# Optimization experiments

Hardware: AMD Instinct MI355X
Metric: run time of the kernel (lower is better)

Reference implementation:

```python
import jax, jax.numpy as jnp
import numpy as np

N, D, H = 524288, 64, 256


def setup_inputs() -> dict:
    key = jax.random.key(0)
    k1, k2, k3 = jax.random.split(key, 3)
    X = jax.random.normal(k1, (N, D), dtype=jnp.float32)
    centers = jax.random.normal(k2, (H, D), dtype=jnp.float32)
    w = jax.random.normal(k3, (1, H), dtype=jnp.float32) / np.sqrt(H)
    b = jnp.zeros((1,), dtype=jnp.float32)
    return {"X": X, "centers": centers, "w": w, "b": b}


def reference(X, centers, w, b):
    # RBF feature map: phi[n, h] = exp(-||X[n] - centers[h]||^2)
    # Squared euclidean distance via the expanded form to avoid the
    # [N, H, D] broadcast intermediate the naive torch version builds.
    x2 = jnp.sum(X * X, axis=-1, keepdims=True)           # [N, 1]
    c2 = jnp.sum(centers * centers, axis=-1)               # [H]
    xc = jnp.einsum('nd,hd->nh', X, centers)               # [N, H]
    d2 = jnp.maximum(x2 - 2.0 * xc + c2[None, :], 0.0)     # [N, H]
    feats = jnp.exp(-d2)                                   # gaussian kernel
    # Linear head: nn.Linear(hidden_dim, 1)
    return feats @ w.T + b                                 # [N, 1]
```

## Files before the change

kernel.cpp:

```cpp
#include <hip/hip_runtime.h>

#define NROWS 524288
#define DDIM  64
#define HCENT 256
#define GRID  512
#define CPB   4

typedef short bf16x8 __attribute__((ext_vector_type(8)));
typedef float f32x4  __attribute__((ext_vector_type(4)));

#define LOG2E 1.4426950408889634f
#define K2L   2.8853900817779268f
#define BIASF 80.0f

__device__ __forceinline__ float fast_exp2(float x) {
#if __has_builtin(__builtin_amdgcn_exp2f)
  return __builtin_amdgcn_exp2f(x);
#else
  return exp2f(x);
#endif
}

__global__ __launch_bounds__(512, 4) void rbf_main(const float* __restrict__ X,
                                                   const float* __restrict__ bptr,
                                                   const float* __restrict__ centers,
                                                   const float* __restrict__ w,
                                                   float* __restrict__ out) {
  __shared__ int4 BH[16 * 2 * 64];
  __shared__ int4 BL[16 * 2 * 64];
  __shared__ float2 CWs[HCENT];

  const int tid  = threadIdx.x;
  const int wave = tid >> 6;
  const int lane = tid & 63;
  const int q    = lane >> 4;
  const int c    = lane & 15;

  float c2acc[2] = {0.f, 0.f};
#pragma unroll
  for (int i = 0; i < 4; ++i) {
    int pair = wave * 4 + i;
    int ct = pair >> 1;
    int kc = pair & 1;
    const float* src = centers + (ct * 16 + c) * DDIM + kc * 32 + q * 8;
    float4 f0 = reinterpret_cast<const float4*>(src)[0];
    float4 f1 = reinterpret_cast<const float4*>(src)[1];
    float xs[8] = {f0.x, f0.y, f0.z, f0.w, f1.x, f1.y, f1.z, f1.w};
    int hp[4], lp[4];
    float part = 0.f;
#pragma unroll
    for (int p = 0; p < 4; ++p) {
      float x0 = xs[2 * p], x1 = xs[2 * p + 1];
      part = fmaf(x0, x0, part);
      part = fmaf(x1, x1, part);
      unsigned u0 = __float_as_uint(x0);
      unsigned u1 = __float_as_uint(x1);
      float l0 = x0 - __uint_as_float(u0 & 0xFFFF0000u);
      float l1 = x1 - __uint_as_float(u1 & 0xFFFF0000u);
      hp[p] = (int)((u1 & 0xFFFF0000u) | (u0 >> 16));
      lp[p] = (int)((__float_as_uint(l1) & 0xFFFF0000u) | (__float_as_uint(l0) >> 16));
    }
    part += __shfl_xor(part, 16, 64);
    part += __shfl_xor(part, 32, 64);
    c2acc[i >> 1] += part;
    int idx = pair * 64 + lane;
    BH[idx] = make_int4(hp[0], hp[1], hp[2], hp[3]);
    BL[idx] = make_int4(lp[0], lp[1], lp[2], lp[3]);
  }
  if (lane < 16) {
#pragma unroll
    for (int t = 0; t < 2; ++t) {
      int h = (wave * 2 + t) * 16 + lane;
      CWs[h] = make_float2(-fmaf(c2acc[t], LOG2E, BIASF), w[h]);
    }
  }

  float bval = bptr[0];

  __syncthreads();

  const bf16x8* BHv = reinterpret_cast<const bf16x8*>(BH);
  const bf16x8* BLv = reinterpret_cast<const bf16x8*>(BL);

#pragma unroll 1
  for (int s = 0; s < CPB; ++s) {
    int rowbase = (blockIdx.x * CPB + s) * 256 + wave * 32;

    bf16x8 ah[2][2], al[2][2];
    float x2p[2];
#pragma unroll
    for (int rt = 0; rt < 2; ++rt) {
      const float* rp = X + (rowbase + rt * 16 + c) * DDIM + q * 8;
      float part = 0.f;
#pragma unroll
      for (int kc = 0; kc < 2; ++kc) {
        float4 f0 = reinterpret_cast<const float4*>(rp + kc * 32)[0];
        float4 f1 = reinterpret_cast<const float4*>(rp + kc * 32)[1];
        float xs[8] = {f0.x, f0.y, f0.z, f0.w, f1.x, f1.y, f1.z, f1.w};
        union { int i[4]; bf16x8 v; } uh, ul;
#pragma unroll
        for (int p = 0; p < 4; ++p) {
          float x0 = xs[2 * p], x1 = xs[2 * p + 1];
          part = fmaf(x0, x0, part);
          part = fmaf(x1, x1, part);
          unsigned u0 = __float_as_uint(x0);
          unsigned u1 = __float_as_uint(x1);
          float l0 = x0 - __uint_as_float(u0 & 0xFFFF0000u);
          float l1 = x1 - __uint_as_float(u1 & 0xFFFF0000u);
          uh.i[p] = (int)((u1 & 0xFFFF0000u) | (u0 >> 16));
          ul.i[p] = (int)((__float_as_uint(l1) & 0xFFFF0000u) | (__float_as_uint(l0) >> 16));
        }
        ah[rt][kc] = uh.v;
        al[rt][kc] = ul.v;
      }
      x2p[rt] = part;
    }

    float psum[2][4] = {{0.f, 0.f, 0.f, 0.f}, {0.f, 0.f, 0.f, 0.f}};
#pragma unroll 2
    for (int ct = 0; ct < 16; ++ct) {
      int idx = ct * 128 + lane;
      bf16x8 bh0 = BHv[idx], bh1 = BHv[idx + 64];
      bf16x8 bl0 = BLv[idx], bl1 = BLv[idx + 64];
      float2 mw = CWs[ct * 16 + c];
#pragma unroll
      for (int rt = 0; rt < 2; ++rt) {
        f32x4 acc = {0.f, 0.f, 0.f, 0.f};
        acc = __builtin_amdgcn_mfma_f32_16x16x32_bf16(ah[rt][0], bh0, acc, 0, 0, 0);
        acc = __builtin_amdgcn_mfma_f32_16x16x32_bf16(ah[rt][1], bh1, acc, 0, 0, 0);
        acc = __builtin_amdgcn_mfma_f32_16x16x32_bf16(al[rt][0], bh0, acc, 0, 0, 0);
        acc = __builtin_amdgcn_mfma_f32_16x16x32_bf16(al[rt][1], bh1, acc, 0, 0, 0);
        acc = __builtin_amdgcn_mfma_f32_16x16x32_bf16(ah[rt][0], bl0, acc, 0, 0, 0);
        acc = __builtin_amdgcn_mfma_f32_16x16x32_bf16(ah[rt][1], bl1, acc, 0, 0, 0);
#pragma unroll
        for (int r = 0; r < 4; ++r) {
          float e = fast_exp2(fmaf(acc[r], K2L, mw.x));
          psum[rt][r] = fmaf(e, mw.y, psum[rt][r]);
        }
      }
    }

#pragma unroll
    for (int rt = 0; rt < 2; ++rt) {
      float part = x2p[rt];
      part += __shfl_xor(part, 16, 64);
      part += __shfl_xor(part, 32, 64);
#pragma unroll
      for (int r = 0; r < 4; ++r) {
        float v = psum[rt][r];
        v += __shfl_xor(v, 1, 64);
        v += __shfl_xor(v, 2, 64);
        v += __shfl_xor(v, 4, 64);
        v += __shfl_xor(v, 8, 64);
        float x2row = __shfl(part, q * 4 + r, 64);
        float rowf = fast_exp2(fmaf(-LOG2E, x2row, BIASF));
        psum[rt][r] = fmaf(v, rowf, bval);
      }
      if (c == 0) {
        float4 o = make_float4(psum[rt][0], psum[rt][1], psum[rt][2], psum[rt][3]);
        *reinterpret_cast<float4*>(out + rowbase + rt * 16 + q * 4) = o;
      }
    }
  }
}

extern "C" void kernel_launch(void* const* d_in, const int* in_sizes, int n_in,
                              void* d_out, int out_size, void* d_ws, size_t ws_size,
                              hipStream_t stream) {
  const float* X       = (const float*)d_in[0];
  const float* centers = (const float*)d_in[1];
  const float* w       = (const float*)d_in[2];
  const float* b       = (const float*)d_in[3];
  float* out = (float*)d_out;
  (void)d_ws; (void)ws_size;

  rbf_main<<<GRID, 512, 0, stream>>>(X, b, centers, w, out);
}
```

Before: 206.4 us.

## Switch to single fp16 MFMA pass and software-prefetch next row chunk

Replaces the split-bf16 three-term emulation (hi*hi, lo*hi, hi*lo, six MFMAs per tile) with a single fp16 conversion of X and centers, two MFMAs per tile. This drops the low-part LDS buffer and its conversion work. It also unrolls the four chunks and double-buffers the raw X loads, so the next chunk's global loads overlap the current chunk's compute. fp16 loses mantissa bits versus the split scheme and can overflow for large inputs, which risks accuracy in the exponent of the gaussian.

```diff
diff --git a/kernel.cpp b/kernel.cpp
--- a/kernel.cpp
+++ b/kernel.cpp
@@ -6,8 +6,8 @@
 #define GRID  512
 #define CPB   4
 
-typedef short bf16x8 __attribute__((ext_vector_type(8)));
-typedef float f32x4  __attribute__((ext_vector_type(4)));
+typedef _Float16 half8 __attribute__((ext_vector_type(8)));
+typedef float    f32x4 __attribute__((ext_vector_type(4)));
 
 #define LOG2E 1.4426950408889634f
 #define K2L   2.8853900817779268f
@@ -25,9 +25,104 @@
                                                    const float* __restrict__ bptr,
                                                    const float* __restrict__ centers,
                                                    const float* __restrict__ w,
+                                                   float* __restrict__ out);
+
+__device__ __forceinline__ void load_chunk(const float* __restrict__ X, int rowbase,
+                                           int c, int q, float4 (&raw)[8]) {
+#pragma unroll
+  for (int rt = 0; rt < 2; ++rt) {
+    const float* rp = X + (rowbase + rt * 16 + c) * DDIM + q * 8;
+#pragma unroll
+    for (int kc = 0; kc < 2; ++kc) {
+      raw[rt * 4 + kc * 2 + 0] = reinterpret_cast<const float4*>(rp + kc * 32)[0];
+      raw[rt * 4 + kc * 2 + 1] = reinterpret_cast<const float4*>(rp + kc * 32)[1];
+    }
+  }
+}
+
+__device__ __forceinline__ void convert_chunk(const float4 (&raw)[8],
+                                              half8 (&a)[2][2], float (&x2p)[2]) {
+#pragma unroll
+  for (int rt = 0; rt < 2; ++rt) {
+    float part = 0.f;
+#pragma unroll
+    for (int kc = 0; kc < 2; ++kc) {
+      const float4 f0 = raw[rt * 4 + kc * 2 + 0];
+      const float4 f1 = raw[rt * 4 + kc * 2 + 1];
+      const float xs[8] = {f0.x, f0.y, f0.z, f0.w, f1.x, f1.y, f1.z, f1.w};
+      union { _Float16 h[8]; half8 v; } u;
+#pragma unroll
+      for (int p = 0; p < 8; ++p) {
+        part = fmaf(xs[p], xs[p], part);
+        u.h[p] = (_Float16)xs[p];
+      }
+      a[rt][kc] = u.v;
+    }
+    x2p[rt] = part;
+  }
+}
+
+__device__ __forceinline__ void chunk_body(const float* __restrict__ X, int rowbase,
+                                           bool prefetch,
+                                           const float4 (&cur)[8], float4 (&nxt)[8],
+                                           const half8* __restrict__ BHv,
+                                           const float2* __restrict__ CWs,
+                                           int lane, int q, int c, float bval,
+                                           float* __restrict__ out) {
+  if (prefetch) load_chunk(X, rowbase + 256, c, q, nxt);
+
+  half8 a[2][2];
+  float x2p[2];
+  convert_chunk(cur, a, x2p);
+
+  float psum[2][4] = {{0.f, 0.f, 0.f, 0.f}, {0.f, 0.f, 0.f, 0.f}};
+#pragma unroll 2
+  for (int ct = 0; ct < 16; ++ct) {
+    int idx = ct * 128 + lane;
+    half8 bh0 = BHv[idx], bh1 = BHv[idx + 64];
+    float2 mw = CWs[ct * 16 + c];
+#pragma unroll
+    for (int rt = 0; rt < 2; ++rt) {
+      f32x4 acc = {0.f, 0.f, 0.f, 0.f};
+      acc = __builtin_amdgcn_mfma_f32_16x16x32_f16(a[rt][0], bh0, acc, 0, 0, 0);
+      acc = __builtin_amdgcn_mfma_f32_16x16x32_f16(a[rt][1], bh1, acc, 0, 0, 0);
+#pragma unroll
+      for (int r = 0; r < 4; ++r) {
+        float e = fast_exp2(fmaf(acc[r], K2L, mw.x));
+        psum[rt][r] = fmaf(e, mw.y, psum[rt][r]);
+      }
+    }
+  }
+
+#pragma unroll
+  for (int rt = 0; rt < 2; ++rt) {
+    float part = x2p[rt];
+    part += __shfl_xor(part, 16, 64);
+    part += __shfl_xor(part, 32, 64);
+#pragma unroll
+    for (int r = 0; r < 4; ++r) {
+      float v = psum[rt][r];
+      v += __shfl_xor(v, 1, 64);
+      v += __shfl_xor(v, 2, 64);
+      v += __shfl_xor(v, 4, 64);
+      v += __shfl_xor(v, 8, 64);
+      float x2row = __shfl(part, q * 4 + r, 64);
+      float rowf = fast_exp2(fmaf(-LOG2E, x2row, BIASF));
+      psum[rt][r] = fmaf(v, rowf, bval);
+    }
+    if (c == 0) {
+      float4 o = make_float4(psum[rt][0], psum[rt][1], psum[rt][2], psum[rt][3]);
+      *reinterpret_cast<float4*>(out + rowbase + rt * 16 + q * 4) = o;
+    }
+  }
+}
+
+__global__ __launch_bounds__(512, 4) void rbf_main(const float* __restrict__ X,
+                                                   const float* __restrict__ bptr,
+                                                   const float* __restrict__ centers,
+                                                   const float* __restrict__ w,
                                                    float* __restrict__ out) {
   __shared__ int4 BH[16 * 2 * 64];
-  __shared__ int4 BL[16 * 2 * 64];
   __shared__ float2 CWs[HCENT];
 
   const int tid  = threadIdx.x;
@@ -45,27 +140,18 @@
     const float* src = centers + (ct * 16 + c) * DDIM + kc * 32 + q * 8;
     float4 f0 = reinterpret_cast<const float4*>(src)[0];
     float4 f1 = reinterpret_cast<const float4*>(src)[1];
-    float xs[8] = {f0.x, f0.y, f0.z, f0.w, f1.x, f1.y, f1.z, f1.w};
-    int hp[4], lp[4];
+    const float xs[8] = {f0.x, f0.y, f0.z, f0.w, f1.x, f1.y, f1.z, f1.w};
+    union { _Float16 h[8]; int4 i4; } u;
     float part = 0.f;
 #pragma unroll
-    for (int p = 0; p < 4; ++p) {
-      float x0 = xs[2 * p], x1 = xs[2 * p + 1];
-      part = fmaf(x0, x0, part);
-      part = fmaf(x1, x1, part);
-      unsigned u0 = __float_as_uint(x0);
-      unsigned u1 = __float_as_uint(x1);
-      float l0 = x0 - __uint_as_float(u0 & 0xFFFF0000u);
-      float l1 = x1 - __uint_as_float(u1 & 0xFFFF0000u);
-      hp[p] = (int)((u1 & 0xFFFF0000u) | (u0 >> 16));
-      lp[p] = (int)((__float_as_uint(l1) & 0xFFFF0000u) | (__float_as_uint(l0) >> 16));
+    for (int p = 0; p < 8; ++p) {
+      part = fmaf(xs[p], xs[p], part);
+      u.h[p] = (_Float16)xs[p];
     }
     part += __shfl_xor(part, 16, 64);
     part += __shfl_xor(part, 32, 64);
     c2acc[i >> 1] += part;
-    int idx = pair * 64 + lane;
-    BH[idx] = make_int4(hp[0], hp[1], hp[2], hp[3]);
-    BL[idx] = make_int4(lp[0], lp[1], lp[2], lp[3]);
+    BH[pair * 64 + lane] = u.i4;
   }
   if (lane < 16) {
 #pragma unroll
@@ -79,89 +165,17 @@
 
   __syncthreads();
 
-  const bf16x8* BHv = reinterpret_cast<const bf16x8*>(BH);
-  const bf16x8* BLv = reinterpret_cast<const bf16x8*>(BL);
+  const half8* BHv = reinterpret_cast<const half8*>(BH);
 
-#pragma unroll 1
-  for (int s = 0; s < CPB; ++s) {
-    int rowbase = (blockIdx.x * CPB + s) * 256 + wave * 32;
+  const int rb0 = blockIdx.x * CPB * 256 + wave * 32;
 
-    bf16x8 ah[2][2], al[2][2];
-    float x2p[2];
-#pragma unroll
-    for (int rt = 0; rt < 2; ++rt) {
-      const float* rp = X + (rowbase + rt * 16 + c) * DDIM + q * 8;
-      float part = 0.f;
-#pragma unroll
-      for (int kc = 0; kc < 2; ++kc) {
-        float4 f0 = reinterpret_cast<const float4*>(rp + kc * 32)[0];
-        float4 f1 = reinterpret_cast<const float4*>(rp + kc * 32)[1];
-        float xs[8] = {f0.x, f0.y, f0.z, f0.w, f1.x, f1.y, f1.z, f1.w};
-        union { int i[4]; bf16x8 v; } uh, ul;
-#pragma unroll
-        for (int p = 0; p < 4; ++p) {
-          float x0 = xs[2 * p], x1 = xs[2 * p + 1];
-          part = fmaf(x0, x0, part);
-          part = fmaf(x1, x1, part);
-          unsigned u0 = __float_as_uint(x0);
-          unsigned u1 = __float_as_uint(x1);
-          float l0 = x0 - __uint_as_float(u0 & 0xFFFF0000u);
-          float l1 = x1 - __uint_as_float(u1 & 0xFFFF0000u);
-          uh.i[p] = (int)((u1 & 0xFFFF0000u) | (u0 >> 16));
-          ul.i[p] = (int)((__float_as_uint(l1) & 0xFFFF0000u) | (__float_as_uint(l0) >> 16));
-        }
-        ah[rt][kc] = uh.v;
-        al[rt][kc] = ul.v;
-      }
-      x2p[rt] = part;
-    }
+  float4 rawA[8], rawB[8];
+  load_chunk(X, rb0, c, q, rawA);
 
-    float psum[2][4] = {{0.f, 0.f, 0.f, 0.f}, {0.f, 0.f, 0.f, 0.f}};
-#pragma unroll 2
-    for (int ct = 0; ct < 16; ++ct) {
-      int idx = ct * 128 + lane;
-      bf16x8 bh0 = BHv[idx], bh1 = BHv[idx + 64];
-      bf16x8 bl0 = BLv[idx], bl1 = BLv[idx + 64];
-      float2 mw = CWs[ct * 16 + c];
-#pragma unroll
-      for (int rt = 0; rt < 2; ++rt) {
-        f32x4 acc = {0.f, 0.f, 0.f, 0.f};
-        acc = __builtin_amdgcn_mfma_f32_16x16x32_bf16(ah[rt][0], bh0, acc, 0, 0, 0);
-        acc = __builtin_amdgcn_mfma_f32_16x16x32_bf16(ah[rt][1], bh1, acc, 0, 0, 0);
-        acc = __builtin_amdgcn_mfma_f32_16x16x32_bf16(al[rt][0], bh0, acc, 0, 0, 0);
-        acc = __builtin_amdgcn_mfma_f32_16x16x32_bf16(al[rt][1], bh1, acc, 0, 0, 0);
-        acc = __builtin_amdgcn_mfma_f32_16x16x32_bf16(ah[rt][0], bl0, acc, 0, 0, 0);
-        acc = __builtin_amdgcn_mfma_f32_16x16x32_bf16(ah[rt][1], bl1, acc, 0, 0, 0);
-#pragma unroll
-        for (int r = 0; r < 4; ++r) {
-          float e = fast_exp2(fmaf(acc[r], K2L, mw.x));
-          psum[rt][r] = fmaf(e, mw.y, psum[rt][r]);
-        }
-      }
-    }
-
-#pragma unroll
-    for (int rt = 0; rt < 2; ++rt) {
-      float part = x2p[rt];
-      part += __shfl_xor(part, 16, 64);
-      part += __shfl_xor(part, 32, 64);
-#pragma unroll
-      for (int r = 0; r < 4; ++r) {
-        float v = psum[rt][r];
-        v += __shfl_xor(v, 1, 64);
-        v += __shfl_xor(v, 2, 64);
-        v += __shfl_xor(v, 4, 64);
-        v += __shfl_xor(v, 8, 64);
-        float x2row = __shfl(part, q * 4 + r, 64);
-        float rowf = fast_exp2(fmaf(-LOG2E, x2row, BIASF));
-        psum[rt][r] = fmaf(v, rowf, bval);
-      }
-      if (c == 0) {
-        float4 o = make_float4(psum[rt][0], psum[rt][1], psum[rt][2], psum[rt][3]);
-        *reinterpret_cast<float4*>(out + rowbase + rt * 16 + q * 4) = o;
-      }
-    }
-  }
+  chunk_body(X, rb0 + 0 * 256, true,  rawA, rawB, BHv, CWs, lane, q, c, bval, out);
+  chunk_body(X, rb0 + 1 * 256, true,  rawB, rawA, BHv, CWs, lane, q, c, bval, out);
+  chunk_body(X, rb0 + 2 * 256, true,  rawA, rawB, BHv, CWs, lane, q, c, bval, out);
+  chunk_body(X, rb0 + 3 * 256, false, rawB, rawA, BHv, CWs, lane, q, c, bval, out);
 }
 
 extern "C" void kernel_launch(void* const* d_in, const int* in_sizes, int n_in,
```

Result: no change. 205.0 us (-0.7%).
